# Kernel optimization log

Measured on AMD Instinct MI355X. Metric: run time of the kernel, lower is better.

## Reference

```python
import jax, jax.numpy as jnp
import numpy as np

B, T, D = 2048, 100, 128
HID = [512, 256, 128]
ALPHA, NOISE_STD = 0.2, 0.05


def _lin_init(key, fan_in, fan_out):
    k1, k2 = jax.random.split(key)
    b = 1.0 / np.sqrt(fan_in)
    W = jax.random.uniform(k1, (fan_in, fan_out), minval=-b, maxval=b, dtype=jnp.float32)
    bias = jax.random.uniform(k2, (fan_out,), minval=-b, maxval=b, dtype=jnp.float32)
    return W, bias


def setup_inputs() -> dict:
    key = jax.random.key(0)
    ks = jax.random.split(key, 10)
    x = jax.random.normal(ks[0], (B, T, D), dtype=jnp.float32)
    noise = jax.random.normal(ks[1], (B, T - 1, HID[-1]), dtype=jnp.float32)
    e_w0, e_b0 = _lin_init(ks[2], D, HID[0])
    e_w1, e_b1 = _lin_init(ks[3], HID[0], HID[1])
    e_w2, e_b2 = _lin_init(ks[4], HID[1], HID[2])
    d_w0, d_b0 = _lin_init(ks[5], HID[2], HID[1])
    d_w1, d_b1 = _lin_init(ks[6], HID[1], HID[0])
    d_w2, d_b2 = _lin_init(ks[7], HID[0], D)
    m = jax.random.normal(ks[8], (HID[-1], 2), dtype=jnp.float32)
    n = jax.random.normal(ks[9], (HID[-1], 2), dtype=jnp.float32)
    return {"x": x, "noise": noise, "seq_len": T,
            "e_w0": e_w0, "e_b0": e_b0, "e_w1": e_w1, "e_b1": e_b1,
            "e_w2": e_w2, "e_b2": e_b2, "d_w0": d_w0, "d_b0": d_b0,
            "d_w1": d_w1, "d_b1": d_b1, "d_w2": d_w2, "d_b2": d_b2,
            "m": m, "n": n}


def reference(x, noise, seq_len, e_w0, e_b0, e_w1, e_b1, e_w2, e_b2,
              d_w0, d_b0, d_w1, d_b1, d_w2, d_b2, m, n):
    hs = m.shape[0]  # latent size (128)
    x = jnp.where(jnp.isnan(x), 0.0, x)  # NaN masking as in Autoencoder.forward

    def encoder(v):
        v = jax.nn.relu(v @ e_w0 + e_b0)
        v = jax.nn.relu(v @ e_w1 + e_b1)
        return v @ e_w2 + e_b2

    def decoder(v):
        v = jax.nn.relu(v @ d_w0 + d_b0)
        v = jax.nn.relu(v @ d_w1 + d_b1)
        return v @ d_w2 + d_b2

    h_enc = encoder(x)              # (B, T, hs)
    x_reconstruct = decoder(h_enc)  # (B, T, D)
    h0 = h_enc[:, 0, :]             # (B, hs)
    x0 = x[:, 0, :]                 # (B, D)

    def step(h, nz):
        r = jnp.tanh(h)
        # low-rank recurrence: rank-2 update m n^T / hidden_size
        dh = ALPHA * (-h + (r @ n) @ m.T / hs) + NOISE_STD * nz
        h = h + dh
        out = decoder(jnp.tanh(h))
        return h, (h, out)

    _, (zs, outs) = jax.lax.scan(step, h0, jnp.swapaxes(noise, 0, 1))
    z_pred = jnp.concatenate([h0[:, None, :], jnp.swapaxes(zs, 0, 1)], axis=1)
    x_pred = jnp.concatenate([x0[:, None, :], jnp.swapaxes(outs, 0, 1)], axis=1)
    return x_pred, x_reconstruct, z_pred
```

## Files before the change

### kernel.cpp

```cpp
#include <hip/hip_runtime.h>
#include <math.h>

namespace {

constexpr int B_  = 2048;
constexpr int T_  = 100;
constexpr int D_  = 128;
constexpr int BT_ = B_ * T_;
constexpr int M_  = 64;

using f32x4  = __attribute__((ext_vector_type(4))) float;
using bf16x8 = __attribute__((ext_vector_type(8))) __bf16;

enum { MODE_ENC = 0, MODE_ID = 1, MODE_TANH = 2 };

__device__ __forceinline__ unsigned short f2bf(float f) {
  unsigned int u = __float_as_uint(f);
  return (unsigned short)((u + 0x7FFFu + ((u >> 16) & 1u)) >> 16);
}
__device__ __forceinline__ unsigned int pack2(float a, float b) {
  return (unsigned int)f2bf(a) | ((unsigned int)f2bf(b) << 16);
}
__device__ __forceinline__ float ftanh(float x) {
  const float e = __expf(2.0f * x);
  return 1.0f - 2.0f / (e + 1.0f);
}

template <int KGEMM, int NT, int KFW>
__device__ __forceinline__ void gemm(const char* __restrict__ A, const int astr,
                                     const unsigned short* __restrict__ Wt,
                                     f32x4 (&acc)[NT][4], const int lrow, const int lk) {
  constexpr int NK = KGEMM / 32;
  const int key = lrow << 4;
  const unsigned short* wl = Wt + lk * 8;
#pragma unroll
  for (int kk = 0; kk < NK; ++kk) {
    int4 breg[NT];
#pragma unroll
    for (int nt = 0; nt < NT; ++nt)
      breg[nt] = *reinterpret_cast<const int4*>(
          wl + (size_t)(nt * 16 + lrow) * KFW + kk * 32);
    bf16x8 act[4];
#pragma unroll
    for (int s = 0; s < 4; ++s)
      act[s] = __builtin_bit_cast(bf16x8,
          *reinterpret_cast<const int4*>(A + (lrow + s * 16) * astr + ((kk * 64 + lk * 16) ^ key)));
#pragma unroll
    for (int nt = 0; nt < NT; ++nt) {
      const bf16x8 w = __builtin_bit_cast(bf16x8, breg[nt]);
#pragma unroll
      for (int s = 0; s < 4; ++s)
        acc[nt][s] = __builtin_amdgcn_mfma_f32_16x16x32_bf16(w, act[s], acc[nt][s], 0, 0, 0);
    }
  }
}

template <int NT>
__device__ __forceinline__ void init_bias(f32x4 (&acc)[NT][4], const float* __restrict__ bias,
                                          const int lk) {
#pragma unroll
  for (int nt = 0; nt < NT; ++nt) {
    const f32x4 bv = *reinterpret_cast<const f32x4*>(bias + nt * 16 + lk * 4);
#pragma unroll
    for (int s = 0; s < 4; ++s) acc[nt][s] = bv;
  }
}

template <int NT, bool RELU>
__device__ __forceinline__ void store_lds_pk(char* __restrict__ dst, const int strideB,
                                             const int colLocal0, f32x4 (&acc)[NT][4],
                                             const int lrow, const int lk) {
  const int key = lrow << 4;
#pragma unroll
  for (int nt = 0; nt < NT; ++nt) {
    const int colb = (colLocal0 + nt * 16 + lk * 4) * 2;
#pragma unroll
    for (int s = 0; s < 4; ++s) {
      float v0 = acc[nt][s][0], v1 = acc[nt][s][1], v2 = acc[nt][s][2], v3 = acc[nt][s][3];
      if (RELU) {
        v0 = fmaxf(v0, 0.f); v1 = fmaxf(v1, 0.f); v2 = fmaxf(v2, 0.f); v3 = fmaxf(v3, 0.f);
      }
      uint2 w;
      w.x = pack2(v0, v1);
      w.y = pack2(v2, v3);
      *reinterpret_cast<uint2*>(dst + (s * 16 + lrow) * strideB + (colb ^ key)) = w;
    }
  }
}

template <int MODE>
__device__ __forceinline__ int rowmap(const int rl) {
  if constexpr (MODE == MODE_TANH) {
    const int b = rl / 99;
    return b * T_ + (rl - b * 99) + 1;
  }
  return rl;
}

template <int MODE>
__device__ __forceinline__ void store_global(float* __restrict__ gout, f32x4 (&acc)[1][4],
                                             const int r0, const int col0,
                                             const int lrow, const int lk) {
#pragma unroll
  for (int s = 0; s < 4; ++s) {
    const int g = rowmap<MODE>(r0 + s * 16 + lrow);
    *reinterpret_cast<float4*>(gout + (size_t)g * D_ + col0 + lk * 4) =
        __builtin_bit_cast(float4, acc[0][s]);
  }
}

template <int MODE>
__device__ __forceinline__ void stage(const float* __restrict__ in, char* __restrict__ X,
                                      float* __restrict__ xpred0,
                                      const int r0, const int tid) {
#pragma unroll
  for (int i = 0; i < 2; ++i) {
    const int c   = tid + i * 512;
    const int row = c >> 4;
    const int cb  = c & 15;
    const int rl  = r0 + row;
    const int g   = rowmap<MODE>(rl);
    const float4* gp = reinterpret_cast<const float4*>(in + (size_t)g * D_ + cb * 8);
    float4 v0 = gp[0], v1 = gp[1];
    if constexpr (MODE == MODE_ENC) {
      v0.x = (v0.x == v0.x) ? v0.x : 0.f;  v0.y = (v0.y == v0.y) ? v0.y : 0.f;
      v0.z = (v0.z == v0.z) ? v0.z : 0.f;  v0.w = (v0.w == v0.w) ? v0.w : 0.f;
      v1.x = (v1.x == v1.x) ? v1.x : 0.f;  v1.y = (v1.y == v1.y) ? v1.y : 0.f;
      v1.z = (v1.z == v1.z) ? v1.z : 0.f;  v1.w = (v1.w == v1.w) ? v1.w : 0.f;
      if (rl % T_ == 0) {
        float4* xp = reinterpret_cast<float4*>(xpred0 + (size_t)g * D_ + cb * 8);
        xp[0] = v0; xp[1] = v1;
      }
    }
    if constexpr (MODE == MODE_TANH) {
      v0.x = ftanh(v0.x); v0.y = ftanh(v0.y); v0.z = ftanh(v0.z); v0.w = ftanh(v0.w);
      v1.x = ftanh(v1.x); v1.y = ftanh(v1.y); v1.z = ftanh(v1.z); v1.w = ftanh(v1.w);
    }
    int4 pk;
    pk.x = (int)pack2(v0.x, v0.y); pk.y = (int)pack2(v0.z, v0.w);
    pk.z = (int)pack2(v1.x, v1.y); pk.w = (int)pack2(v1.z, v1.w);
    *reinterpret_cast<int4*>(X + row * 256 + ((cb * 16) ^ ((row & 15) << 4))) = pk;
  }
}

template <int MODE>
__device__ __forceinline__ void dec_body(const unsigned short* __restrict__ dW0t, const float* __restrict__ d_b0,
                                         const unsigned short* __restrict__ dW1t, const float* __restrict__ d_b1,
                                         const unsigned short* __restrict__ dW2t, const float* __restrict__ d_b2,
                                         float* __restrict__ gout,
                                         char* __restrict__ Aa, char* __restrict__ Bs,
                                         const int r0, const int wave, const int lrow, const int lk) {
  f32x4 acc1[2][4];
  init_bias<2>(acc1, d_b0 + wave * 32, lk);
  gemm<128, 2, 128>(Bs, 256, dW0t + (size_t)(wave * 32) * 128, acc1, lrow, lk);
  store_lds_pk<2, true>(Aa, 512, wave * 32, acc1, lrow, lk);
  __syncthreads();

  f32x4 acc3[1][4];
  init_bias<1>(acc3, d_b2 + wave * 16, lk);
#pragma unroll
  for (int g = 0; g < 2; ++g) {
    f32x4 acc2[2][4];
    init_bias<2>(acc2, d_b1 + g * 256 + wave * 32, lk);
    gemm<256, 2, 256>(Aa, 512, dW1t + (size_t)(g * 256 + wave * 32) * 256, acc2, lrow, lk);
    if (g) __syncthreads();
    store_lds_pk<2, true>(Bs, 512, wave * 32, acc2, lrow, lk);
    __syncthreads();
    gemm<256, 1, 512>(Bs, 512, dW2t + (size_t)(wave * 16) * 512 + g * 256, acc3, lrow, lk);
  }
  store_global<MODE>(gout, acc3, r0, wave * 16, lrow, lk);
}

__launch_bounds__(512, 4)
__global__ void enc_dec_kernel(const float* __restrict__ in,
                               const unsigned short* __restrict__ eW0t, const float* __restrict__ e_b0,
                               const unsigned short* __restrict__ eW1t, const float* __restrict__ e_b1,
                               const unsigned short* __restrict__ eW2t, const float* __restrict__ e_b2,
                               const unsigned short* __restrict__ dW0t, const float* __restrict__ d_b0,
                               const unsigned short* __restrict__ dW1t, const float* __restrict__ d_b1,
                               const unsigned short* __restrict__ dW2t, const float* __restrict__ d_b2,
                               float* __restrict__ z, float* __restrict__ x_rec,
                               float* __restrict__ x_pred) {
  __shared__ __align__(16) char Aa[M_ * 512];
  __shared__ __align__(16) char Bs[M_ * 512];

  const int tid  = threadIdx.x;
  const int wave = tid >> 6;
  const int lane = tid & 63;
  const int lrow = lane & 15;
  const int lk   = lane >> 4;
  const int r0   = blockIdx.x * M_;

  stage<MODE_ENC>(in, Aa, x_pred, r0, tid);
  __syncthreads();

  f32x4 acc2[2][4];
  init_bias<2>(acc2, e_b1 + wave * 32, lk);
#pragma unroll
  for (int h = 0; h < 2; ++h) {
    f32x4 acc1[2][4];
    init_bias<2>(acc1, e_b0 + h * 256 + wave * 32, lk);
    gemm<128, 2, 128>(Aa, 256, eW0t + (size_t)(h * 256 + wave * 32) * 128, acc1, lrow, lk);
    if (h) __syncthreads();
    store_lds_pk<2, true>(Bs, 512, wave * 32, acc1, lrow, lk);
    __syncthreads();
    gemm<256, 2, 512>(Bs, 512, eW1t + (size_t)(wave * 32) * 512 + h * 256, acc2, lrow, lk);
  }
  store_lds_pk<2, true>(Aa, 512, wave * 32, acc2, lrow, lk);
  __syncthreads();

  f32x4 acc3[1][4];
  init_bias<1>(acc3, e_b2 + wave * 16, lk);
  gemm<256, 1, 256>(Aa, 512, eW2t + (size_t)(wave * 16) * 256, acc3, lrow, lk);
  store_lds_pk<1, false>(Bs, 256, wave * 16, acc3, lrow, lk);
  store_global<MODE_ENC>(z, acc3, r0, wave * 16, lrow, lk);
  __syncthreads();

  dec_body<MODE_ID>(dW0t, d_b0, dW1t, d_b1, dW2t, d_b2, x_rec, Aa, Bs, r0, wave, lrow, lk);
}

__launch_bounds__(512, 4)
__global__ void pred_dec_kernel(const float* __restrict__ zin,
                                const unsigned short* __restrict__ dW0t, const float* __restrict__ d_b0,
                                const unsigned short* __restrict__ dW1t, const float* __restrict__ d_b1,
                                const unsigned short* __restrict__ dW2t, const float* __restrict__ d_b2,
                                float* __restrict__ x_pred) {
  __shared__ __align__(16) char Aa[M_ * 512];
  __shared__ __align__(16) char Bs[M_ * 512];

  const int tid  = threadIdx.x;
  const int wave = tid >> 6;
  const int lane = tid & 63;
  const int lrow = lane & 15;
  const int lk   = lane >> 4;
  const int r0   = blockIdx.x * M_;

  stage<MODE_TANH>(zin, Bs, nullptr, r0, tid);
  __syncthreads();
  dec_body<MODE_TANH>(dW0t, d_b0, dW1t, d_b1, dW2t, d_b2, x_pred, Aa, Bs, r0, wave, lrow, lk);
}

__global__ void wprep_all_kernel(const float* __restrict__ s0, const float* __restrict__ s1,
                                 const float* __restrict__ s2, const float* __restrict__ s3,
                                 const float* __restrict__ s4, const float* __restrict__ s5,
                                 unsigned short* __restrict__ d0, unsigned short* __restrict__ d1,
                                 unsigned short* __restrict__ d2, unsigned short* __restrict__ d3,
                                 unsigned short* __restrict__ d4, unsigned short* __restrict__ d5) {
  const int id = blockIdx.x * blockDim.x + threadIdx.x;
  const float* src; unsigned short* dst; int K, N, l;
  if (id < 65536)       { src = s0; dst = d0; K = 128; N = 512; l = id; }
  else if (id < 196608) { src = s1; dst = d1; K = 512; N = 256; l = id - 65536; }
  else if (id < 229376) { src = s2; dst = d2; K = 256; N = 128; l = id - 196608; }
  else if (id < 262144) { src = s3; dst = d3; K = 128; N = 256; l = id - 229376; }
  else if (id < 393216) { src = s4; dst = d4; K = 256; N = 512; l = id - 262144; }
  else                  { src = s5; dst = d5; K = 512; N = 128; l = id - 393216; }
  const int k = l / N;
  const int n = l - k * N;
  dst[(size_t)n * K + k] = f2bf(src[l]);
}

__global__ void rnn_scan_kernel(const float* __restrict__ noise,
                                const float* __restrict__ m, const float* __restrict__ n,
                                float* __restrict__ z) {
  const int gtid = blockIdx.x * blockDim.x + threadIdx.x;
  const int b = gtid >> 6;
  const int lane = threadIdx.x & 63;
  const int k0 = lane, k1 = lane + 64;

  const float mk00 = m[k0 * 2], mk01 = m[k0 * 2 + 1];
  const float mk10 = m[k1 * 2], mk11 = m[k1 * 2 + 1];
  const float nk00 = n[k0 * 2], nk01 = n[k0 * 2 + 1];
  const float nk10 = n[k1 * 2], nk11 = n[k1 * 2 + 1];

  float* zb = z + (size_t)b * T_ * D_;
  const float* nzb = noise + (size_t)b * (T_ - 1) * D_;
  float h0 = zb[k0];
  float h1 = zb[k1];

#pragma unroll 1
  for (int t = 0; t < T_ - 1; ++t) {
    const float r0v = tanhf(h0);
    const float r1v = tanhf(h1);
    float p0 = r0v * nk00 + r1v * nk10;
    float p1 = r0v * nk01 + r1v * nk11;
#pragma unroll
    for (int off = 32; off > 0; off >>= 1) {
      p0 += __shfl_xor(p0, off);
      p1 += __shfl_xor(p1, off);
    }
    const float v0 = (p0 * mk00 + p1 * mk01) * (1.0f / 128.0f);
    const float v1 = (p0 * mk10 + p1 * mk11) * (1.0f / 128.0f);
    const float nz0 = nzb[t * D_ + k0];
    const float nz1 = nzb[t * D_ + k1];
    h0 += 0.2f * (v0 - h0) + 0.05f * nz0;
    h1 += 0.2f * (v1 - h1) + 0.05f * nz1;
    zb[(t + 1) * D_ + k0] = h0;
    zb[(t + 1) * D_ + k1] = h1;
  }
}

}

extern "C" void kernel_launch(void* const* d_in, const int* in_sizes, int n_in,
                              void* d_out, int out_size, void* d_ws, size_t ws_size,
                              hipStream_t stream) {
  (void)in_sizes; (void)n_in; (void)ws_size; (void)out_size;

  const float* x     = (const float*)d_in[0];
  const float* noise = (const float*)d_in[1];
  const float* e_w0 = (const float*)d_in[3];
  const float* e_b0 = (const float*)d_in[4];
  const float* e_w1 = (const float*)d_in[5];
  const float* e_b1 = (const float*)d_in[6];
  const float* e_w2 = (const float*)d_in[7];
  const float* e_b2 = (const float*)d_in[8];
  const float* d_w0 = (const float*)d_in[9];
  const float* d_b0 = (const float*)d_in[10];
  const float* d_w1 = (const float*)d_in[11];
  const float* d_b1 = (const float*)d_in[12];
  const float* d_w2 = (const float*)d_in[13];
  const float* d_b2 = (const float*)d_in[14];
  const float* m    = (const float*)d_in[15];
  const float* n    = (const float*)d_in[16];

  float* out    = (float*)d_out;
  float* x_pred = out;
  float* x_rec  = out + (size_t)BT_ * D_;
  float* z      = out + 2 * (size_t)BT_ * D_;

  unsigned short* ws = (unsigned short*)d_ws;
  unsigned short* eW0t = ws;
  unsigned short* eW1t = ws + 65536;
  unsigned short* eW2t = ws + 196608;
  unsigned short* dW0t = ws + 229376;
  unsigned short* dW1t = ws + 262144;
  unsigned short* dW2t = ws + 393216;

  wprep_all_kernel<<<458752 / 256, 256, 0, stream>>>(e_w0, e_w1, e_w2, d_w0, d_w1, d_w2,
                                                     eW0t, eW1t, eW2t, dW0t, dW1t, dW2t);

  enc_dec_kernel<<<BT_ / M_, 512, 0, stream>>>(x,
      eW0t, e_b0, eW1t, e_b1, eW2t, e_b2,
      dW0t, d_b0, dW1t, d_b1, dW2t, d_b2,
      z, x_rec, x_pred);

  rnn_scan_kernel<<<B_ / 4, 256, 0, stream>>>(noise, m, n, z);

  pred_dec_kernel<<<(B_ * (T_ - 1)) / M_, 512, 0, stream>>>(z,
      dW0t, d_b0, dW1t, d_b1, dW2t, d_b2, x_pred);
}
```

Baseline: 665.2 us.

## Switch GEMM tiles from 16x16x32 to 32x32x16 MFMA instructions

```diff
diff --git a/kernel.cpp b/kernel.cpp
--- a/kernel.cpp
+++ b/kernel.cpp
@@ -10,6 +10,7 @@
 constexpr int M_  = 64;
 
 using f32x4  = __attribute__((ext_vector_type(4))) float;
+using f32x16 = __attribute__((ext_vector_type(16))) float;
 using bf16x8 = __attribute__((ext_vector_type(8))) __bf16;
 
 enum { MODE_ENC = 0, MODE_ID = 1, MODE_TANH = 2 };
@@ -26,64 +27,61 @@
   return 1.0f - 2.0f / (e + 1.0f);
 }
 
-template <int KGEMM, int NT, int KFW>
-__device__ __forceinline__ void gemm(const char* __restrict__ A, const int astr,
-                                     const unsigned short* __restrict__ Wt,
-                                     f32x4 (&acc)[NT][4], const int lrow, const int lk) {
-  constexpr int NK = KGEMM / 32;
-  const int key = lrow << 4;
-  const unsigned short* wl = Wt + lk * 8;
+template <int KGEMM, int NSUB, int KFW>
+__device__ __forceinline__ void gemm32(const char* __restrict__ A, const int astr,
+                                       const unsigned short* __restrict__ Wt,
+                                       f32x16 (&acc)[NSUB], const int rowbase,
+                                       const int l31, const int hi) {
+  constexpr int NK = KGEMM / 16;
+  const int key = (l31 & 15) << 4;
+  const unsigned short* wl = Wt + (size_t)l31 * KFW + hi * 8;
 #pragma unroll
   for (int kk = 0; kk < NK; ++kk) {
-    int4 breg[NT];
-#pragma unroll
-    for (int nt = 0; nt < NT; ++nt)
-      breg[nt] = *reinterpret_cast<const int4*>(
-          wl + (size_t)(nt * 16 + lrow) * KFW + kk * 32);
-    bf16x8 act[4];
-#pragma unroll
-    for (int s = 0; s < 4; ++s)
-      act[s] = __builtin_bit_cast(bf16x8,
-          *reinterpret_cast<const int4*>(A + (lrow + s * 16) * astr + ((kk * 64 + lk * 16) ^ key)));
-#pragma unroll
-    for (int nt = 0; nt < NT; ++nt) {
-      const bf16x8 w = __builtin_bit_cast(bf16x8, breg[nt]);
-#pragma unroll
-      for (int s = 0; s < 4; ++s)
-        acc[nt][s] = __builtin_amdgcn_mfma_f32_16x16x32_bf16(w, act[s], acc[nt][s], 0, 0, 0);
-    }
-  }
-}
-
-template <int NT>
-__device__ __forceinline__ void init_bias(f32x4 (&acc)[NT][4], const float* __restrict__ bias,
-                                          const int lk) {
-#pragma unroll
-  for (int nt = 0; nt < NT; ++nt) {
-    const f32x4 bv = *reinterpret_cast<const f32x4*>(bias + nt * 16 + lk * 4);
-#pragma unroll
-    for (int s = 0; s < 4; ++s) acc[nt][s] = bv;
-  }
-}
-
-template <int NT, bool RELU>
-__device__ __forceinline__ void store_lds_pk(char* __restrict__ dst, const int strideB,
-                                             const int colLocal0, f32x4 (&acc)[NT][4],
-                                             const int lrow, const int lk) {
-  const int key = lrow << 4;
-#pragma unroll
-  for (int nt = 0; nt < NT; ++nt) {
-    const int colb = (colLocal0 + nt * 16 + lk * 4) * 2;
-#pragma unroll
-    for (int s = 0; s < 4; ++s) {
-      float v0 = acc[nt][s][0], v1 = acc[nt][s][1], v2 = acc[nt][s][2], v3 = acc[nt][s][3];
+    const int4 wr = *reinterpret_cast<const int4*>(wl + kk * 16);
+    const bf16x8 w = __builtin_bit_cast(bf16x8, wr);
+#pragma unroll
+    for (int s = 0; s < NSUB; ++s) {
+      const int row = rowbase + s * 32 + l31;
+      const int4 ar = *reinterpret_cast<const int4*>(A + row * astr + ((kk * 32 + hi * 16) ^ key));
+      acc[s] = __builtin_amdgcn_mfma_f32_32x32x16_bf16(w, __builtin_bit_cast(bf16x8, ar), acc[s], 0, 0, 0);
+    }
+  }
+}
+
+template <int NSUB>
+__device__ __forceinline__ void init_bias32(f32x16 (&acc)[NSUB], const float* __restrict__ bias,
+                                            const int hi) {
+#pragma unroll
+  for (int g4 = 0; g4 < 4; ++g4) {
+    const f32x4 bv = *reinterpret_cast<const f32x4*>(bias + g4 * 8 + hi * 4);
+#pragma unroll
+    for (int j = 0; j < 4; ++j)
+#pragma unroll
+      for (int s = 0; s < NSUB; ++s) acc[s][g4 * 4 + j] = bv[j];
+  }
+}
+
+template <int NSUB, bool RELU>
+__device__ __forceinline__ void store_lds_pk32(char* __restrict__ dst, const int strideB,
+                                               const int colLocal0, f32x16 (&acc)[NSUB],
+                                               const int rowbase, const int l31, const int hi) {
+#pragma unroll
+  for (int s = 0; s < NSUB; ++s) {
+    const int ar = rowbase + s * 32 + l31;
+    const int key = (ar & 15) << 4;
+    char* drow = dst + ar * strideB;
+#pragma unroll
+    for (int g4 = 0; g4 < 4; ++g4) {
+      float v0 = acc[s][g4 * 4 + 0], v1 = acc[s][g4 * 4 + 1];
+      float v2 = acc[s][g4 * 4 + 2], v3 = acc[s][g4 * 4 + 3];
       if (RELU) {
         v0 = fmaxf(v0, 0.f); v1 = fmaxf(v1, 0.f); v2 = fmaxf(v2, 0.f); v3 = fmaxf(v3, 0.f);
       }
       uint2 w;
       w.x = pack2(v0, v1);
       w.y = pack2(v2, v3);
-      *reinterpret_cast<uint2*>(dst + (s * 16 + lrow) * strideB + (colb ^ key)) = w;
+      const int colb = (colLocal0 + hi * 4 + g4 * 8) * 2;
+      *reinterpret_cast<uint2*>(drow + (colb ^ key)) = w;
     }
   }
 }
@@ -98,14 +96,16 @@
 }
 
 template <int MODE>
-__device__ __forceinline__ void store_global(float* __restrict__ gout, f32x4 (&acc)[1][4],
-                                             const int r0, const int col0,
-                                             const int lrow, const int lk) {
-#pragma unroll
-  for (int s = 0; s < 4; ++s) {
-    const int g = rowmap<MODE>(r0 + s * 16 + lrow);
-    *reinterpret_cast<float4*>(gout + (size_t)g * D_ + col0 + lk * 4) =
-        __builtin_bit_cast(float4, acc[0][s]);
+__device__ __forceinline__ void store_global32(float* __restrict__ gout, const f32x16& a,
+                                               const int r0, const int col0,
+                                               const int rowbase, const int l31, const int hi) {
+  const int g = rowmap<MODE>(r0 + rowbase + l31);
+  float* gr = gout + (size_t)g * D_ + col0 + hi * 4;
+#pragma unroll
+  for (int g4 = 0; g4 < 4; ++g4) {
+    float4 v;
+    v.x = a[g4 * 4 + 0]; v.y = a[g4 * 4 + 1]; v.z = a[g4 * 4 + 2]; v.w = a[g4 * 4 + 3];
+    *reinterpret_cast<float4*>(gr + g4 * 8) = v;
   }
 }
 
@@ -149,26 +149,29 @@
                                          const unsigned short* __restrict__ dW2t, const float* __restrict__ d_b2,
                                          float* __restrict__ gout,
                                          char* __restrict__ Aa, char* __restrict__ Bs,
-                                         const int r0, const int wave, const int lrow, const int lk) {
-  f32x4 acc1[2][4];
-  init_bias<2>(acc1, d_b0 + wave * 32, lk);
-  gemm<128, 2, 128>(Bs, 256, dW0t + (size_t)(wave * 32) * 128, acc1, lrow, lk);
-  store_lds_pk<2, true>(Aa, 512, wave * 32, acc1, lrow, lk);
-  __syncthreads();
-
-  f32x4 acc3[1][4];
-  init_bias<1>(acc3, d_b2 + wave * 16, lk);
+                                         const int r0, const int wave, const int l31, const int hi) {
+  const int wc = (wave & 3) * 32;
+  const int wr = (wave >> 2) * 32;
+
+  f32x16 acc1[2];
+  init_bias32<2>(acc1, d_b0 + wave * 32, hi);
+  gemm32<128, 2, 128>(Bs, 256, dW0t + (size_t)(wave * 32) * 128, acc1, 0, l31, hi);
+  store_lds_pk32<2, true>(Aa, 512, wave * 32, acc1, 0, l31, hi);
+  __syncthreads();
+
+  f32x16 acc3[1];
+  init_bias32<1>(acc3, d_b2 + wc, hi);
 #pragma unroll
   for (int g = 0; g < 2; ++g) {
-    f32x4 acc2[2][4];
-    init_bias<2>(acc2, d_b1 + g * 256 + wave * 32, lk);
-    gemm<256, 2, 256>(Aa, 512, dW1t + (size_t)(g * 256 + wave * 32) * 256, acc2, lrow, lk);
+    f32x16 acc2[2];
+    init_bias32<2>(acc2, d_b1 + g * 256 + wave * 32, hi);
+    gemm32<256, 2, 256>(Aa, 512, dW1t + (size_t)(g * 256 + wave * 32) * 256, acc2, 0, l31, hi);
     if (g) __syncthreads();
-    store_lds_pk<2, true>(Bs, 512, wave * 32, acc2, lrow, lk);
+    store_lds_pk32<2, true>(Bs, 512, wave * 32, acc2, 0, l31, hi);
     __syncthreads();
-    gemm<256, 1, 512>(Bs, 512, dW2t + (size_t)(wave * 16) * 512 + g * 256, acc3, lrow, lk);
-  }
-  store_global<MODE>(gout, acc3, r0, wave * 16, lrow, lk);
+    gemm32<256, 1, 512>(Bs, 512, dW2t + (size_t)wc * 512 + g * 256, acc3, wr, l31, hi);
+  }
+  store_global32<MODE>(gout, acc3[0], r0, wc, wr, l31, hi);
 }
 
 __launch_bounds__(512, 4)
@@ -187,36 +190,38 @@
   const int tid  = threadIdx.x;
   const int wave = tid >> 6;
   const int lane = tid & 63;
-  const int lrow = lane & 15;
-  const int lk   = lane >> 4;
+  const int l31  = lane & 31;
+  const int hi   = lane >> 5;
   const int r0   = blockIdx.x * M_;
+  const int wc   = (wave & 3) * 32;
+  const int wr   = (wave >> 2) * 32;
 
   stage<MODE_ENC>(in, Aa, x_pred, r0, tid);
   __syncthreads();
 
-  f32x4 acc2[2][4];
-  init_bias<2>(acc2, e_b1 + wave * 32, lk);
+  f32x16 acc2[2];
+  init_bias32<2>(acc2, e_b1 + wave * 32, hi);
 #pragma unroll
   for (int h = 0; h < 2; ++h) {
-    f32x4 acc1[2][4];
-    init_bias<2>(acc1, e_b0 + h * 256 + wave * 32, lk);
-    gemm<128, 2, 128>(Aa, 256, eW0t + (size_t)(h * 256 + wave * 32) * 128, acc1, lrow, lk);
+    f32x16 acc1[2];
+    init_bias32<2>(acc1, e_b0 + h * 256 + wave * 32, hi);
+    gemm32<128, 2, 128>(Aa, 256, eW0t + (size_t)(h * 256 + wave * 32) * 128, acc1, 0, l31, hi);
     if (h) __syncthreads();
-    store_lds_pk<2, true>(Bs, 512, wave * 32, acc1, lrow, lk);
+    store_lds_pk32<2, true>(Bs, 512, wave * 32, acc1, 0, l31, hi);
     __syncthreads();
-    gemm<256, 2, 512>(Bs, 512, eW1t + (size_t)(wave * 32) * 512 + h * 256, acc2, lrow, lk);
-  }
-  store_lds_pk<2, true>(Aa, 512, wave * 32, acc2, lrow, lk);
-  __syncthreads();
-
-  f32x4 acc3[1][4];
-  init_bias<1>(acc3, e_b2 + wave * 16, lk);
-  gemm<256, 1, 256>(Aa, 512, eW2t + (size_t)(wave * 16) * 256, acc3, lrow, lk);
-  store_lds_pk<1, false>(Bs, 256, wave * 16, acc3, lrow, lk);
-  store_global<MODE_ENC>(z, acc3, r0, wave * 16, lrow, lk);
-  __syncthreads();
-
-  dec_body<MODE_ID>(dW0t, d_b0, dW1t, d_b1, dW2t, d_b2, x_rec, Aa, Bs, r0, wave, lrow, lk);
+    gemm32<256, 2, 512>(Bs, 512, eW1t + (size_t)(wave * 32) * 512 + h * 256, acc2, 0, l31, hi);
+  }
+  store_lds_pk32<2, true>(Aa, 512, wave * 32, acc2, 0, l31, hi);
+  __syncthreads();
+
+  f32x16 acc3[1];
+  init_bias32<1>(acc3, e_b2 + wc, hi);
+  gemm32<256, 1, 256>(Aa, 512, eW2t + (size_t)wc * 256, acc3, wr, l31, hi);
+  store_lds_pk32<1, false>(Bs, 256, wc, acc3, wr, l31, hi);
+  store_global32<MODE_ENC>(z, acc3[0], r0, wc, wr, l31, hi);
+  __syncthreads();
+
+  dec_body<MODE_ID>(dW0t, d_b0, dW1t, d_b1, dW2t, d_b2, x_rec, Aa, Bs, r0, wave, l31, hi);
 }
 
 __launch_bounds__(512, 4)
@@ -231,13 +236,13 @@
   const int tid  = threadIdx.x;
   const int wave = tid >> 6;
   const int lane = tid & 63;
-  const int lrow = lane & 15;
-  const int lk   = lane >> 4;
+  const int l31  = lane & 31;
+  const int hi   = lane >> 5;
   const int r0   = blockIdx.x * M_;
 
   stage<MODE_TANH>(zin, Bs, nullptr, r0, tid);
   __syncthreads();
-  dec_body<MODE_TANH>(dW0t, d_b0, dW1t, d_b1, dW2t, d_b2, x_pred, Aa, Bs, r0, wave, lrow, lk);
+  dec_body<MODE_TANH>(dW0t, d_b0, dW1t, d_b1, dW2t, d_b2, x_pred, Aa, Bs, r0, wave, l31, hi);
 }
 
 __global__ void wprep_all_kernel(const float* __restrict__ s0, const float* __restrict__ s1,
```

Result: slower. 828.8 us (+24.6%).

## Retile wave work as 2x4 grid over rows and columns in MLP GEMMs

Applied to the files above, without the earlier changes.

```diff
diff --git a/kernel.cpp b/kernel.cpp
--- a/kernel.cpp
+++ b/kernel.cpp
@@ -26,10 +26,11 @@
   return 1.0f - 2.0f / (e + 1.0f);
 }
 
-template <int KGEMM, int NT, int KFW>
+template <int KGEMM, int NT, int NSUB, int KFW>
 __device__ __forceinline__ void gemm(const char* __restrict__ A, const int astr,
                                      const unsigned short* __restrict__ Wt,
-                                     f32x4 (&acc)[NT][4], const int lrow, const int lk) {
+                                     f32x4 (&acc)[NT][NSUB], const int rowbase,
+                                     const int lrow, const int lk) {
   constexpr int NK = KGEMM / 32;
   const int key = lrow << 4;
   const unsigned short* wl = Wt + lk * 8;
@@ -40,42 +41,42 @@
     for (int nt = 0; nt < NT; ++nt)
       breg[nt] = *reinterpret_cast<const int4*>(
           wl + (size_t)(nt * 16 + lrow) * KFW + kk * 32);
-    bf16x8 act[4];
-#pragma unroll
-    for (int s = 0; s < 4; ++s)
+    bf16x8 act[NSUB];
+#pragma unroll
+    for (int s = 0; s < NSUB; ++s)
       act[s] = __builtin_bit_cast(bf16x8,
-          *reinterpret_cast<const int4*>(A + (lrow + s * 16) * astr + ((kk * 64 + lk * 16) ^ key)));
+          *reinterpret_cast<const int4*>(A + (rowbase + s * 16 + lrow) * astr + ((kk * 64 + lk * 16) ^ key)));
 #pragma unroll
     for (int nt = 0; nt < NT; ++nt) {
       const bf16x8 w = __builtin_bit_cast(bf16x8, breg[nt]);
 #pragma unroll
-      for (int s = 0; s < 4; ++s)
+      for (int s = 0; s < NSUB; ++s)
         acc[nt][s] = __builtin_amdgcn_mfma_f32_16x16x32_bf16(w, act[s], acc[nt][s], 0, 0, 0);
     }
   }
 }
 
-template <int NT>
-__device__ __forceinline__ void init_bias(f32x4 (&acc)[NT][4], const float* __restrict__ bias,
+template <int NT, int NSUB>
+__device__ __forceinline__ void init_bias(f32x4 (&acc)[NT][NSUB], const float* __restrict__ bias,
                                           const int lk) {
 #pragma unroll
   for (int nt = 0; nt < NT; ++nt) {
     const f32x4 bv = *reinterpret_cast<const f32x4*>(bias + nt * 16 + lk * 4);
 #pragma unroll
-    for (int s = 0; s < 4; ++s) acc[nt][s] = bv;
-  }
-}
-
-template <int NT, bool RELU>
+    for (int s = 0; s < NSUB; ++s) acc[nt][s] = bv;
+  }
+}
+
+template <int NT, int NSUB, bool RELU>
 __device__ __forceinline__ void store_lds_pk(char* __restrict__ dst, const int strideB,
-                                             const int colLocal0, f32x4 (&acc)[NT][4],
-                                             const int lrow, const int lk) {
+                                             const int colLocal0, f32x4 (&acc)[NT][NSUB],
+                                             const int rowbase, const int lrow, const int lk) {
   const int key = lrow << 4;
 #pragma unroll
   for (int nt = 0; nt < NT; ++nt) {
     const int colb = (colLocal0 + nt * 16 + lk * 4) * 2;
 #pragma unroll
-    for (int s = 0; s < 4; ++s) {
+    for (int s = 0; s < NSUB; ++s) {
       float v0 = acc[nt][s][0], v1 = acc[nt][s][1], v2 = acc[nt][s][2], v3 = acc[nt][s][3];
       if (RELU) {
         v0 = fmaxf(v0, 0.f); v1 = fmaxf(v1, 0.f); v2 = fmaxf(v2, 0.f); v3 = fmaxf(v3, 0.f);
@@ -83,7 +84,7 @@
       uint2 w;
       w.x = pack2(v0, v1);
       w.y = pack2(v2, v3);
-      *reinterpret_cast<uint2*>(dst + (s * 16 + lrow) * strideB + (colb ^ key)) = w;
+      *reinterpret_cast<uint2*>(dst + (rowbase + s * 16 + lrow) * strideB + (colb ^ key)) = w;
     }
   }
 }
@@ -97,15 +98,17 @@
   return rl;
 }
 
-template <int MODE>
-__device__ __forceinline__ void store_global(float* __restrict__ gout, f32x4 (&acc)[1][4],
-                                             const int r0, const int col0,
+template <int MODE, int NT, int NSUB>
+__device__ __forceinline__ void store_global(float* __restrict__ gout, f32x4 (&acc)[NT][NSUB],
+                                             const int r0, const int col0, const int rowbase,
                                              const int lrow, const int lk) {
 #pragma unroll
-  for (int s = 0; s < 4; ++s) {
-    const int g = rowmap<MODE>(r0 + s * 16 + lrow);
-    *reinterpret_cast<float4*>(gout + (size_t)g * D_ + col0 + lk * 4) =
-        __builtin_bit_cast(float4, acc[0][s]);
+  for (int s = 0; s < NSUB; ++s) {
+    const int g = rowmap<MODE>(r0 + rowbase + s * 16 + lrow);
+    float* gr = gout + (size_t)g * D_ + col0 + lk * 4;
+#pragma unroll
+    for (int nt = 0; nt < NT; ++nt)
+      *reinterpret_cast<float4*>(gr + nt * 16) = __builtin_bit_cast(float4, acc[nt][s]);
   }
 }
 
@@ -150,25 +153,28 @@
                                          float* __restrict__ gout,
                                          char* __restrict__ Aa, char* __restrict__ Bs,
                                          const int r0, const int wave, const int lrow, const int lk) {
-  f32x4 acc1[2][4];
-  init_bias<2>(acc1, d_b0 + wave * 32, lk);
-  gemm<128, 2, 128>(Bs, 256, dW0t + (size_t)(wave * 32) * 128, acc1, lrow, lk);
-  store_lds_pk<2, true>(Aa, 512, wave * 32, acc1, lrow, lk);
-  __syncthreads();
-
-  f32x4 acc3[1][4];
-  init_bias<1>(acc3, d_b2 + wave * 16, lk);
+  const int wc = wave & 3;
+  const int wr = (wave >> 2) * 32;
+
+  f32x4 acc1[4][2];
+  init_bias<4, 2>(acc1, d_b0 + wc * 64, lk);
+  gemm<128, 4, 2, 128>(Bs, 256, dW0t + (size_t)(wc * 64) * 128, acc1, wr, lrow, lk);
+  store_lds_pk<4, 2, true>(Aa, 512, wc * 64, acc1, wr, lrow, lk);
+  __syncthreads();
+
+  f32x4 acc3[2][2];
+  init_bias<2, 2>(acc3, d_b2 + wc * 32, lk);
 #pragma unroll
   for (int g = 0; g < 2; ++g) {
-    f32x4 acc2[2][4];
-    init_bias<2>(acc2, d_b1 + g * 256 + wave * 32, lk);
-    gemm<256, 2, 256>(Aa, 512, dW1t + (size_t)(g * 256 + wave * 32) * 256, acc2, lrow, lk);
+    f32x4 acc2[4][2];
+    init_bias<4, 2>(acc2, d_b1 + g * 256 + wc * 64, lk);
+    gemm<256, 4, 2, 256>(Aa, 512, dW1t + (size_t)(g * 256 + wc * 64) * 256, acc2, wr, lrow, lk);
     if (g) __syncthreads();
-    store_lds_pk<2, true>(Bs, 512, wave * 32, acc2, lrow, lk);
+    store_lds_pk<4, 2, true>(Bs, 512, wc * 64, acc2, wr, lrow, lk);
     __syncthreads();
-    gemm<256, 1, 512>(Bs, 512, dW2t + (size_t)(wave * 16) * 512 + g * 256, acc3, lrow, lk);
-  }
-  store_global<MODE>(gout, acc3, r0, wave * 16, lrow, lk);
+    gemm<256, 2, 2, 512>(Bs, 512, dW2t + (size_t)(wc * 32) * 512 + g * 256, acc3, wr, lrow, lk);
+  }
+  store_global<MODE, 2, 2>(gout, acc3, r0, wc * 32, wr, lrow, lk);
 }
 
 __launch_bounds__(512, 4)
@@ -190,30 +196,32 @@
   const int lrow = lane & 15;
   const int lk   = lane >> 4;
   const int r0   = blockIdx.x * M_;
+  const int wc   = wave & 3;
+  const int wr   = (wave >> 2) * 32;
 
   stage<MODE_ENC>(in, Aa, x_pred, r0, tid);
   __syncthreads();
 
-  f32x4 acc2[2][4];
-  init_bias<2>(acc2, e_b1 + wave * 32, lk);
+  f32x4 acc2[4][2];
+  init_bias<4, 2>(acc2, e_b1 + wc * 64, lk);
 #pragma unroll
   for (int h = 0; h < 2; ++h) {
-    f32x4 acc1[2][4];
-    init_bias<2>(acc1, e_b0 + h * 256 + wave * 32, lk);
-    gemm<128, 2, 128>(Aa, 256, eW0t + (size_t)(h * 256 + wave * 32) * 128, acc1, lrow, lk);
+    f32x4 acc1[4][2];
+    init_bias<4, 2>(acc1, e_b0 + h * 256 + wc * 64, lk);
+    gemm<128, 4, 2, 128>(Aa, 256, eW0t + (size_t)(h * 256 + wc * 64) * 128, acc1, wr, lrow, lk);
     if (h) __syncthreads();
-    store_lds_pk<2, true>(Bs, 512, wave * 32, acc1, lrow, lk);
+    store_lds_pk<4, 2, true>(Bs, 512, wc * 64, acc1, wr, lrow, lk);
     __syncthreads();
-    gemm<256, 2, 512>(Bs, 512, eW1t + (size_t)(wave * 32) * 512 + h * 256, acc2, lrow, lk);
-  }
-  store_lds_pk<2, true>(Aa, 512, wave * 32, acc2, lrow, lk);
-  __syncthreads();
-
-  f32x4 acc3[1][4];
-  init_bias<1>(acc3, e_b2 + wave * 16, lk);
-  gemm<256, 1, 256>(Aa, 512, eW2t + (size_t)(wave * 16) * 256, acc3, lrow, lk);
-  store_lds_pk<1, false>(Bs, 256, wave * 16, acc3, lrow, lk);
-  store_global<MODE_ENC>(z, acc3, r0, wave * 16, lrow, lk);
+    gemm<256, 4, 2, 512>(Bs, 512, eW1t + (size_t)(wc * 64) * 512 + h * 256, acc2, wr, lrow, lk);
+  }
+  store_lds_pk<4, 2, true>(Aa, 512, wc * 64, acc2, wr, lrow, lk);
+  __syncthreads();
+
+  f32x4 acc3[2][2];
+  init_bias<2, 2>(acc3, e_b2 + wc * 32, lk);
+  gemm<256, 2, 2, 256>(Aa, 512, eW2t + (size_t)(wc * 32) * 256, acc3, wr, lrow, lk);
+  store_lds_pk<2, 2, false>(Bs, 256, wc * 32, acc3, wr, lrow, lk);
+  store_global<MODE_ENC, 2, 2>(z, acc3, r0, wc * 32, wr, lrow, lk);
   __syncthreads();
 
   dec_body<MODE_ID>(dW0t, d_b0, dW1t, d_b1, dW2t, d_b2, x_rec, Aa, Bs, r0, wave, lrow, lk);
```

After: 1.153 ms. 73.4% more time.

## Stage full 512-wide encoder hidden in LDS and run one K=512 GEMM

Applied to the files above, without the earlier changes.

```diff
diff --git a/kernel.cpp b/kernel.cpp
--- a/kernel.cpp
+++ b/kernel.cpp
@@ -44,7 +44,7 @@
 #pragma unroll
     for (int s = 0; s < 4; ++s)
       act[s] = __builtin_bit_cast(bf16x8,
-          *reinterpret_cast<const int4*>(A + (lrow + s * 16) * astr + ((kk * 64 + lk * 16) ^ key)));
+          *reinterpret_cast<const int4*>(A + (s * 16 + lrow) * astr + ((kk * 64 + lk * 16) ^ key)));
 #pragma unroll
     for (int nt = 0; nt < NT; ++nt) {
       const bf16x8 w = __builtin_bit_cast(bf16x8, breg[nt]);
@@ -148,12 +148,14 @@
                                          const unsigned short* __restrict__ dW1t, const float* __restrict__ d_b1,
                                          const unsigned short* __restrict__ dW2t, const float* __restrict__ d_b2,
                                          float* __restrict__ gout,
-                                         char* __restrict__ Aa, char* __restrict__ Bs,
+                                         char* __restrict__ X, char* __restrict__ Y,
                                          const int r0, const int wave, const int lrow, const int lk) {
+  char* Yhi = Y + 32768;
+
   f32x4 acc1[2][4];
   init_bias<2>(acc1, d_b0 + wave * 32, lk);
-  gemm<128, 2, 128>(Bs, 256, dW0t + (size_t)(wave * 32) * 128, acc1, lrow, lk);
-  store_lds_pk<2, true>(Aa, 512, wave * 32, acc1, lrow, lk);
+  gemm<128, 2, 128>(X, 256, dW0t + (size_t)(wave * 32) * 128, acc1, lrow, lk);
+  store_lds_pk<2, true>(Y, 512, wave * 32, acc1, lrow, lk);
   __syncthreads();
 
   f32x4 acc3[1][4];
@@ -162,11 +164,11 @@
   for (int g = 0; g < 2; ++g) {
     f32x4 acc2[2][4];
     init_bias<2>(acc2, d_b1 + g * 256 + wave * 32, lk);
-    gemm<256, 2, 256>(Aa, 512, dW1t + (size_t)(g * 256 + wave * 32) * 256, acc2, lrow, lk);
+    gemm<256, 2, 256>(Y, 512, dW1t + (size_t)(g * 256 + wave * 32) * 256, acc2, lrow, lk);
     if (g) __syncthreads();
-    store_lds_pk<2, true>(Bs, 512, wave * 32, acc2, lrow, lk);
+    store_lds_pk<2, true>(Yhi, 512, wave * 32, acc2, lrow, lk);
     __syncthreads();
-    gemm<256, 1, 512>(Bs, 512, dW2t + (size_t)(wave * 16) * 512 + g * 256, acc3, lrow, lk);
+    gemm<256, 1, 512>(Yhi, 512, dW2t + (size_t)(wave * 16) * 512 + g * 256, acc3, lrow, lk);
   }
   store_global<MODE>(gout, acc3, r0, wave * 16, lrow, lk);
 }
@@ -181,8 +183,8 @@
                                const unsigned short* __restrict__ dW2t, const float* __restrict__ d_b2,
                                float* __restrict__ z, float* __restrict__ x_rec,
                                float* __restrict__ x_pred) {
-  __shared__ __align__(16) char Aa[M_ * 512];
-  __shared__ __align__(16) char Bs[M_ * 512];
+  __shared__ __align__(16) char X[M_ * 256];
+  __shared__ __align__(16) char Y[M_ * 1024];
 
   const int tid  = threadIdx.x;
   const int wave = tid >> 6;
@@ -191,32 +193,33 @@
   const int lk   = lane >> 4;
   const int r0   = blockIdx.x * M_;
 
-  stage<MODE_ENC>(in, Aa, x_pred, r0, tid);
-  __syncthreads();
-
-  f32x4 acc2[2][4];
-  init_bias<2>(acc2, e_b1 + wave * 32, lk);
+  stage<MODE_ENC>(in, X, x_pred, r0, tid);
+  __syncthreads();
+
 #pragma unroll
   for (int h = 0; h < 2; ++h) {
     f32x4 acc1[2][4];
     init_bias<2>(acc1, e_b0 + h * 256 + wave * 32, lk);
-    gemm<128, 2, 128>(Aa, 256, eW0t + (size_t)(h * 256 + wave * 32) * 128, acc1, lrow, lk);
-    if (h) __syncthreads();
-    store_lds_pk<2, true>(Bs, 512, wave * 32, acc1, lrow, lk);
-    __syncthreads();
-    gemm<256, 2, 512>(Bs, 512, eW1t + (size_t)(wave * 32) * 512 + h * 256, acc2, lrow, lk);
-  }
-  store_lds_pk<2, true>(Aa, 512, wave * 32, acc2, lrow, lk);
+    gemm<128, 2, 128>(X, 256, eW0t + (size_t)(h * 256 + wave * 32) * 128, acc1, lrow, lk);
+    store_lds_pk<2, true>(Y, 1024, h * 256 + wave * 32, acc1, lrow, lk);
+  }
+  __syncthreads();
+
+  f32x4 acc2[2][4];
+  init_bias<2>(acc2, e_b1 + wave * 32, lk);
+  gemm<512, 2, 512>(Y, 1024, eW1t + (size_t)(wave * 32) * 512, acc2, lrow, lk);
+  __syncthreads();
+  store_lds_pk<2, true>(Y, 512, wave * 32, acc2, lrow, lk);
   __syncthreads();
 
   f32x4 acc3[1][4];
   init_bias<1>(acc3, e_b2 + wave * 16, lk);
-  gemm<256, 1, 256>(Aa, 512, eW2t + (size_t)(wave * 16) * 256, acc3, lrow, lk);
-  store_lds_pk<1, false>(Bs, 256, wave * 16, acc3, lrow, lk);
+  gemm<256, 1, 256>(Y, 512, eW2t + (size_t)(wave * 16) * 256, acc3, lrow, lk);
+  store_lds_pk<1, false>(X, 256, wave * 16, acc3, lrow, lk);
   store_global<MODE_ENC>(z, acc3, r0, wave * 16, lrow, lk);
   __syncthreads();
 
-  dec_body<MODE_ID>(dW0t, d_b0, dW1t, d_b1, dW2t, d_b2, x_rec, Aa, Bs, r0, wave, lrow, lk);
+  dec_body<MODE_ID>(dW0t, d_b0, dW1t, d_b1, dW2t, d_b2, x_rec, X, Y, r0, wave, lrow, lk);
 }
 
 __launch_bounds__(512, 4)
@@ -225,8 +228,8 @@
                                 const unsigned short* __restrict__ dW1t, const float* __restrict__ d_b1,
                                 const unsigned short* __restrict__ dW2t, const float* __restrict__ d_b2,
                                 float* __restrict__ x_pred) {
-  __shared__ __align__(16) char Aa[M_ * 512];
-  __shared__ __align__(16) char Bs[M_ * 512];
+  __shared__ __align__(16) char X[M_ * 256];
+  __shared__ __align__(16) char Y[M_ * 1024];
 
   const int tid  = threadIdx.x;
   const int wave = tid >> 6;
@@ -235,9 +238,9 @@
   const int lk   = lane >> 4;
   const int r0   = blockIdx.x * M_;
 
-  stage<MODE_TANH>(zin, Bs, nullptr, r0, tid);
-  __syncthreads();
-  dec_body<MODE_TANH>(dW0t, d_b0, dW1t, d_b1, dW2t, d_b2, x_pred, Aa, Bs, r0, wave, lrow, lk);
+  stage<MODE_TANH>(zin, X, nullptr, r0, tid);
+  __syncthreads();
+  dec_body<MODE_TANH>(dW0t, d_b0, dW1t, d_b1, dW2t, d_b2, x_pred, X, Y, r0, wave, lrow, lk);
 }
 
 __global__ void wprep_all_kernel(const float* __restrict__ s0, const float* __restrict__ s1,
```

After: 676.7 us. No clear change (+1.7%).
